# Optimization experiments

Hardware: AMD Instinct MI355X
Metric: run time of the kernel (lower is better)

## Reference

```python
import jax, jax.numpy as jnp
import numpy as np

P = 0.5          # dropout-style keep probability (wandb.config.probability)
Z = 1000         # number of Monte-Carlo normal draws in the original loop


def setup_inputs() -> dict:
    key = jax.random.key(0)
    k1, k2, k3 = jax.random.split(key, 3)
    B, D_in, H, C = 65536, 28 * 28, 256, 10
    x = jax.random.uniform(k1, (B, D_in), dtype=jnp.float32)          # pixel-like inputs in [0,1)
    W1 = jax.random.normal(k2, (H, D_in), dtype=jnp.float32) * 0.05   # fc1.weight
    W2 = jax.random.normal(k3, (C, H), dtype=jnp.float32) * 0.05      # fc2.weight
    return {"x": x, "W1": W1, "W2": W2}


def _mc_normal_layer(x, W, key):
    """Gaussian-dropout moment-propagation layer.

    Original torch code draws Z independent Normal(mean, std) samples and
    averages them, which is exactly Normal(mean, std / sqrt(Z)). We use the
    closed form: one eps draw instead of Z kernel launches.
    """
    mean = P * jnp.matmul(x, W.T)                                   # [B, out]
    var = P * (1.0 - P) * jnp.matmul(x * x, (W * W).T)              # [B, out]
    std = jnp.sqrt(var)
    eps = jax.random.normal(key, mean.shape, dtype=mean.dtype)
    return mean + std * (eps / jnp.sqrt(jnp.asarray(Z, mean.dtype)))


def reference(x, W1, W2):
    x = x.reshape(-1, 28 * 28)
    k1, k2 = jax.random.split(jax.random.key(42))
    h = jax.nn.relu(_mc_normal_layer(x, W1, k1))   # [B, H]
    out = _mc_normal_layer(h, W2, k2)              # [B, 10]
    return out
```

## Files before the change

### kernel.cpp

```cpp
#include <hip/hip_runtime.h>
#include <hip/hip_bf16.h>
#include <cstdint>


#define K_DIM 784
#define KP 800
#define N_HID 256
#define N_OUT 10
#define BM 64
#define NSTEP 25
#define WSQ_OFF (N_HID * KP)
#define W2_OFF (832 * 1024)
#define W2SQ 4096
#define H_OFF (1 << 20)
#define BM2 128

using short8 = __attribute__((ext_vector_type(8))) short;
using floatx4 = __attribute__((ext_vector_type(4))) float;
typedef uint16_t u16;

__host__ __device__ inline void threefry2x32(uint32_t k0, uint32_t k1,
                                             uint32_t x0, uint32_t x1,
                                             uint32_t& o0, uint32_t& o1) {
  uint32_t ks0 = k0, ks1 = k1, ks2 = k0 ^ k1 ^ 0x1BD11BDAu;
  x0 += ks0;
  x1 += ks1;
#define TFR(r) { x0 += x1; x1 = (x1 << (r)) | (x1 >> (32 - (r))); x1 ^= x0; }
  TFR(13) TFR(15) TFR(26) TFR(6)   x0 += ks1; x1 += ks2 + 1u;
  TFR(17) TFR(29) TFR(16) TFR(24)  x0 += ks2; x1 += ks0 + 2u;
  TFR(13) TFR(15) TFR(26) TFR(6)   x0 += ks0; x1 += ks1 + 3u;
  TFR(17) TFR(29) TFR(16) TFR(24)  x0 += ks1; x1 += ks2 + 4u;
  TFR(13) TFR(15) TFR(26) TFR(6)   x0 += ks2; x1 += ks0 + 5u;
#undef TFR
  o0 = x0;
  o1 = x1;
}

__device__ __forceinline__ float bits_to_normal(uint32_t bits) {
  const float lo = -0.99999994f;
  float u01 = __uint_as_float((bits >> 9) | 0x3F800000u) - 1.0f;
  float u = fmaxf(lo, u01 * 2.0f + lo);
  float w = -__logf((1.0f - u) * (1.0f + u));
  float p;
  if (w < 5.0f) {
    w -= 2.5f;
    p = 2.81022636e-08f;
    p = fmaf(p, w, 3.43273939e-07f);
    p = fmaf(p, w, -3.5233877e-06f);
    p = fmaf(p, w, -4.39150654e-06f);
    p = fmaf(p, w, 0.00021858087f);
    p = fmaf(p, w, -0.00125372503f);
    p = fmaf(p, w, -0.00417768164f);
    p = fmaf(p, w, 0.246640727f);
    p = fmaf(p, w, 1.50140941f);
  } else {
    w = sqrtf(w) - 3.0f;
    p = -0.000200214257f;
    p = fmaf(p, w, 0.000100950558f);
    p = fmaf(p, w, 0.00134934322f);
    p = fmaf(p, w, -0.00367342844f);
    p = fmaf(p, w, 0.00573950773f);
    p = fmaf(p, w, -0.0076224613f);
    p = fmaf(p, w, 0.00943887047f);
    p = fmaf(p, w, 1.00167406f);
    p = fmaf(p, w, 2.83297682f);
  }
  return 1.41421356f * (p * u);
}

__device__ __forceinline__ float eps_part(uint32_t ka, uint32_t kb, uint32_t i) {
  uint32_t o0, o1;
  threefry2x32(ka, kb, 0u, i, o0, o1);
  return bits_to_normal(o0 ^ o1);
}

__device__ __forceinline__ u16 cvt_bf16(float f) {
  union { __hip_bfloat16 h; u16 u; } c;
  c.h = __float2bfloat16(f);
  return c.u;
}

__device__ __forceinline__ float bf2f(u16 b) {
  return __uint_as_float((uint32_t)b << 16);
}

__global__ __launch_bounds__(256) void pack_w1(const float* __restrict__ W1,
                                               u16* __restrict__ bp) {
  const int col = blockIdx.x;
  for (int k = threadIdx.x; k < KP; k += 256) {
    float w = (k < K_DIM) ? W1[col * K_DIM + k] : 0.0f;
    bp[col * KP + k] = cvt_bf16(w);
    bp[WSQ_OFF + col * KP + k] = cvt_bf16(w * w);
  }
}

__global__ __launch_bounds__(256) void pack_w2(const float* __restrict__ W2,
                                               u16* __restrict__ w2p) {
#pragma unroll
  for (int i = 0; i < 16; ++i) {
    int g = threadIdx.x + i * 256;
    int col = g >> 8, k = g & 255;
    float w = (col < N_OUT) ? W2[col * N_HID + k] : 0.0f;
    w2p[g] = cvt_bf16(w);
    w2p[W2SQ + g] = cvt_bf16(w * w);
  }
}

__global__ __launch_bounds__(256, 4) void gemm1(
    const float* __restrict__ x, const u16* __restrict__ bp,
    u16* __restrict__ hws, uint32_t k1a, uint32_t k1b) {
  __shared__ u16 sA[2][2][BM * 32];

  const int tid = threadIdx.x;
  const int lane = tid & 63;
  const int l15 = lane & 15;
  const int lhal = lane >> 4;
  const int wn = tid >> 6;
  const int bid = blockIdx.x;
  const int gr0 = (bid >> 1) * BM;
  const int bc0 = (bid & 1) * 128;

  const int srow = tid >> 2;
  const int skq = (tid & 3) * 8;
  const float* xptr = x + (size_t)(gr0 + srow) * K_DIM + skq;
  const int sidx = (srow * 32 + skq) ^ ((srow & 7) << 3);

  const uint32_t boff0 = (uint32_t)(bc0 + wn * 32 + 0 * 16 + l15) * KP + (uint32_t)lhal * 8;
  const uint32_t boff1 = (uint32_t)(bc0 + wn * 32 + 1 * 16 + l15) * KP + (uint32_t)lhal * 8;

#define AIDX(i) ((((i * 16 + l15) * 32 + lhal * 8)) ^ (((i * 16 + l15) & 7) << 3))
  const int aidx0 = AIDX(0);
  const int aidx1 = AIDX(1);
  const int aidx2 = AIDX(2);
  const int aidx3 = AIDX(3);
#undef AIDX

#define DECL_ACC(i) \
  floatx4 am##i##0 = {0.f, 0.f, 0.f, 0.f}, am##i##1 = {0.f, 0.f, 0.f, 0.f}; \
  floatx4 av##i##0 = {0.f, 0.f, 0.f, 0.f}, av##i##1 = {0.f, 0.f, 0.f, 0.f};
  DECL_ACC(0) DECL_ACC(1) DECL_ACC(2) DECL_ACC(3)
#undef DECL_ACC

  short8 bm0P, bm1P, bv0P, bv1P;
  short8 bm0Q, bm1Q, bv0Q, bv1Q;
#define LOADB(S, KK) do { \
    const u16* bpk_ = bp + (KK); \
    bm0##S = *reinterpret_cast<const short8*>(&bpk_[boff0]); \
    bm1##S = *reinterpret_cast<const short8*>(&bpk_[boff1]); \
    bv0##S = *reinterpret_cast<const short8*>(&bpk_[WSQ_OFF + boff0]); \
    bv1##S = *reinterpret_cast<const short8*>(&bpk_[WSQ_OFF + boff1]); \
  } while (0)

  float4 q0, q1;
  auto loadX = [&](int kk) {
    if (kk + skq + 8 <= K_DIM) {
      q0 = *reinterpret_cast<const float4*>(xptr + kk);
      q1 = *reinterpret_cast<const float4*>(xptr + kk + 4);
    } else {
      q0 = make_float4(0.f, 0.f, 0.f, 0.f);
      q1 = make_float4(0.f, 0.f, 0.f, 0.f);
    }
  };
  auto writeA = [&](int buf) {
    short8 va, v2;
    va[0] = (short)cvt_bf16(q0.x); v2[0] = (short)cvt_bf16(q0.x * q0.x);
    va[1] = (short)cvt_bf16(q0.y); v2[1] = (short)cvt_bf16(q0.y * q0.y);
    va[2] = (short)cvt_bf16(q0.z); v2[2] = (short)cvt_bf16(q0.z * q0.z);
    va[3] = (short)cvt_bf16(q0.w); v2[3] = (short)cvt_bf16(q0.w * q0.w);
    va[4] = (short)cvt_bf16(q1.x); v2[4] = (short)cvt_bf16(q1.x * q1.x);
    va[5] = (short)cvt_bf16(q1.y); v2[5] = (short)cvt_bf16(q1.y * q1.y);
    va[6] = (short)cvt_bf16(q1.z); v2[6] = (short)cvt_bf16(q1.z * q1.z);
    va[7] = (short)cvt_bf16(q1.w); v2[7] = (short)cvt_bf16(q1.w * q1.w);
    *reinterpret_cast<short8*>(&sA[buf][0][sidx]) = va;
    *reinterpret_cast<short8*>(&sA[buf][1][sidx]) = v2;
  };

#define KSTEP(S_, CUR, NXT, LAST) do { \
    const int kk_ = (S_) * 32; \
    if (!(LAST)) { loadX(kk_ + 32); LOADB(NXT, kk_ + 32); } \
    const u16* sc0_ = &sA[(S_) & 1][0][0]; \
    const u16* sc1_ = &sA[(S_) & 1][1][0]; \
    { \
      const short8 af0_ = *reinterpret_cast<const short8*>(&sc0_[aidx0]); \
      const short8 ag0_ = *reinterpret_cast<const short8*>(&sc1_[aidx0]); \
      const short8 af1_ = *reinterpret_cast<const short8*>(&sc0_[aidx1]); \
      const short8 ag1_ = *reinterpret_cast<const short8*>(&sc1_[aidx1]); \
      const short8 af2_ = *reinterpret_cast<const short8*>(&sc0_[aidx2]); \
      const short8 ag2_ = *reinterpret_cast<const short8*>(&sc1_[aidx2]); \
      const short8 af3_ = *reinterpret_cast<const short8*>(&sc0_[aidx3]); \
      const short8 ag3_ = *reinterpret_cast<const short8*>(&sc1_[aidx3]); \
      am00 = __builtin_amdgcn_mfma_f32_16x16x32_bf16(af0_, bm0##CUR, am00, 0, 0, 0); \
      av00 = __builtin_amdgcn_mfma_f32_16x16x32_bf16(ag0_, bv0##CUR, av00, 0, 0, 0); \
      am01 = __builtin_amdgcn_mfma_f32_16x16x32_bf16(af0_, bm1##CUR, am01, 0, 0, 0); \
      av01 = __builtin_amdgcn_mfma_f32_16x16x32_bf16(ag0_, bv1##CUR, av01, 0, 0, 0); \
      am10 = __builtin_amdgcn_mfma_f32_16x16x32_bf16(af1_, bm0##CUR, am10, 0, 0, 0); \
      av10 = __builtin_amdgcn_mfma_f32_16x16x32_bf16(ag1_, bv0##CUR, av10, 0, 0, 0); \
      am11 = __builtin_amdgcn_mfma_f32_16x16x32_bf16(af1_, bm1##CUR, am11, 0, 0, 0); \
      av11 = __builtin_amdgcn_mfma_f32_16x16x32_bf16(ag1_, bv1##CUR, av11, 0, 0, 0); \
      am20 = __builtin_amdgcn_mfma_f32_16x16x32_bf16(af2_, bm0##CUR, am20, 0, 0, 0); \
      av20 = __builtin_amdgcn_mfma_f32_16x16x32_bf16(ag2_, bv0##CUR, av20, 0, 0, 0); \
      am21 = __builtin_amdgcn_mfma_f32_16x16x32_bf16(af2_, bm1##CUR, am21, 0, 0, 0); \
      av21 = __builtin_amdgcn_mfma_f32_16x16x32_bf16(ag2_, bv1##CUR, av21, 0, 0, 0); \
      am30 = __builtin_amdgcn_mfma_f32_16x16x32_bf16(af3_, bm0##CUR, am30, 0, 0, 0); \
      av30 = __builtin_amdgcn_mfma_f32_16x16x32_bf16(ag3_, bv0##CUR, av30, 0, 0, 0); \
      am31 = __builtin_amdgcn_mfma_f32_16x16x32_bf16(af3_, bm1##CUR, am31, 0, 0, 0); \
      av31 = __builtin_amdgcn_mfma_f32_16x16x32_bf16(ag3_, bv1##CUR, av31, 0, 0, 0); \
    } \
    if (!(LAST)) writeA(((S_) & 1) ^ 1); \
    __syncthreads(); \
  } while (0)

  loadX(0);
  writeA(0);
  LOADB(P, 0);
  __syncthreads();

  for (int s = 0; s < 24; s += 2) {
    KSTEP(s, P, Q, false);
    KSTEP(s + 1, Q, P, false);
  }
  KSTEP(24, P, Q, true);
#undef KSTEP
#undef LOADB

  const float INV = 0.031622776601683794f;
#define EPIG(AM, AV, G, I, J) do { \
    const int rl_ = I * 16 + lhal * 4 + (G); \
    const int c_ = bc0 + wn * 32 + J * 16 + l15; \
    float mean_ = 0.5f * (AM)[G]; \
    float sd_ = 0.5f * sqrtf((AV)[G]); \
    uint32_t idx_ = (uint32_t)(gr0 + rl_) * 256u + (uint32_t)c_; \
    float eps_ = eps_part(k1a, k1b, idx_); \
    float h_ = fmaxf(mean_ + sd_ * (eps_ * INV), 0.0f); \
    hws[(size_t)(gr0 + rl_) * 256 + c_] = cvt_bf16(h_); \
  } while (0)
#define EPI(i, j) do { \
    EPIG(am##i##j, av##i##j, 0, i, j); \
    EPIG(am##i##j, av##i##j, 1, i, j); \
    EPIG(am##i##j, av##i##j, 2, i, j); \
    EPIG(am##i##j, av##i##j, 3, i, j); \
  } while (0)
  EPI(0, 0); EPI(0, 1); EPI(1, 0); EPI(1, 1);
  EPI(2, 0); EPI(2, 1); EPI(3, 0); EPI(3, 1);
#undef EPI
#undef EPIG
}

__global__ __launch_bounds__(256, 4) void layer2(
    const u16* __restrict__ hws, const u16* __restrict__ w2p,
    float* __restrict__ out, uint32_t k2a, uint32_t k2b) {
  __shared__ u16 sH[2][BM2 * 32];

  const int tid = threadIdx.x;
  const int lane = tid & 63;
  const int l15 = lane & 15;
  const int lhal = lane >> 4;
  const int wv = tid >> 6;
  const int gr0 = blockIdx.x * BM2;

  const int srow = tid >> 1;
  const int sq = (tid & 1) * 16;
  const u16* hrow = hws + (size_t)(gr0 + srow) * 256 + sq;
  const int sidx0 = (srow * 32 + sq) ^ ((srow & 7) << 3);
  const int sidx1 = (srow * 32 + sq + 8) ^ ((srow & 7) << 3);

  const uint32_t boff = (uint32_t)l15 * 256 + (uint32_t)lhal * 8;

#define AIDX2(i) ((((wv * 32 + i * 16 + l15) * 32 + lhal * 8)) ^ (((wv * 32 + i * 16 + l15) & 7) << 3))
  const int aidx0 = AIDX2(0);
  const int aidx1 = AIDX2(1);
#undef AIDX2

  floatx4 am0 = {0.f, 0.f, 0.f, 0.f}, am1 = {0.f, 0.f, 0.f, 0.f};
  floatx4 av0 = {0.f, 0.f, 0.f, 0.f}, av1 = {0.f, 0.f, 0.f, 0.f};

  for (int s = 0; s < 8; ++s) {
    __syncthreads();
    const short8 c0 = *reinterpret_cast<const short8*>(&hrow[s * 32]);
    const short8 c1 = *reinterpret_cast<const short8*>(&hrow[s * 32 + 8]);
    short8 s0, s1;
#define SQE(D, S, E) { const float f_ = bf2f((u16)(S)[E]); (D)[E] = (short)cvt_bf16(f_ * f_); }
    SQE(s0, c0, 0) SQE(s0, c0, 1) SQE(s0, c0, 2) SQE(s0, c0, 3)
    SQE(s0, c0, 4) SQE(s0, c0, 5) SQE(s0, c0, 6) SQE(s0, c0, 7)
    SQE(s1, c1, 0) SQE(s1, c1, 1) SQE(s1, c1, 2) SQE(s1, c1, 3)
    SQE(s1, c1, 4) SQE(s1, c1, 5) SQE(s1, c1, 6) SQE(s1, c1, 7)
#undef SQE
    *reinterpret_cast<short8*>(&sH[0][sidx0]) = c0;
    *reinterpret_cast<short8*>(&sH[0][sidx1]) = c1;
    *reinterpret_cast<short8*>(&sH[1][sidx0]) = s0;
    *reinterpret_cast<short8*>(&sH[1][sidx1]) = s1;
    __syncthreads();

    const short8 bm = *reinterpret_cast<const short8*>(&w2p[boff + s * 32]);
    const short8 bv = *reinterpret_cast<const short8*>(&w2p[W2SQ + boff + s * 32]);
    const short8 af0 = *reinterpret_cast<const short8*>(&sH[0][aidx0]);
    const short8 af1 = *reinterpret_cast<const short8*>(&sH[0][aidx1]);
    const short8 ag0 = *reinterpret_cast<const short8*>(&sH[1][aidx0]);
    const short8 ag1 = *reinterpret_cast<const short8*>(&sH[1][aidx1]);
    am0 = __builtin_amdgcn_mfma_f32_16x16x32_bf16(af0, bm, am0, 0, 0, 0);
    av0 = __builtin_amdgcn_mfma_f32_16x16x32_bf16(ag0, bv, av0, 0, 0, 0);
    am1 = __builtin_amdgcn_mfma_f32_16x16x32_bf16(af1, bm, am1, 0, 0, 0);
    av1 = __builtin_amdgcn_mfma_f32_16x16x32_bf16(ag1, bv, av1, 0, 0, 0);
  }

  const float INV = 0.031622776601683794f;
  if (l15 < N_OUT) {
#define L2E(I, G) do { \
    const int row_ = gr0 + wv * 32 + I * 16 + lhal * 4 + (G); \
    float mean_ = 0.5f * am##I[G]; \
    float sd_ = 0.5f * sqrtf(av##I[G]); \
    float eps_ = eps_part(k2a, k2b, (uint32_t)row_ * 10u + (uint32_t)l15); \
    out[(size_t)row_ * 10 + l15] = mean_ + sd_ * (eps_ * INV); \
  } while (0)
    L2E(0, 0); L2E(0, 1); L2E(0, 2); L2E(0, 3);
    L2E(1, 0); L2E(1, 1); L2E(1, 2); L2E(1, 3);
#undef L2E
  }
}

extern "C" void kernel_launch(void* const* d_in, const int* in_sizes, int n_in,
                              void* d_out, int out_size, void* d_ws, size_t ws_size,
                              hipStream_t stream) {
  const float* x = (const float*)d_in[0];
  const float* W1 = (const float*)d_in[1];
  const float* W2 = (const float*)d_in[2];
  float* outp = (float*)d_out;
  u16* bp = (u16*)d_ws;
  u16* w2p = (u16*)((char*)d_ws + W2_OFF);
  u16* hws = (u16*)((char*)d_ws + H_OFF);

  uint32_t k1a, k1b, k2a, k2b;
  threefry2x32(0u, 42u, 0u, 0u, k1a, k1b);
  threefry2x32(0u, 42u, 0u, 1u, k2a, k2b);

  pack_w1<<<256, 256, 0, stream>>>(W1, bp);
  pack_w2<<<1, 256, 0, stream>>>(W2, w2p);
  gemm1<<<(65536 / BM) * 2, 256, 0, stream>>>(x, bp, hws, k1a, k1b);
  layer2<<<65536 / BM2, 256, 0, stream>>>(hws, w2p, outp, k2a, k2b);
}
```

Before: 158.8 us.

## Precompute layer-1 Gaussian noise in separate fp16 kernel before GEMM

Moves the threefry plus inverse-erf noise generation for the hidden layer out of the GEMM epilogue into a standalone rng1 kernel. That kernel packs the noise as fp16 into workspace in the same lane order the epilogue reads, so the GEMM only loads 16-byte vectors. The aim is to shorten the compute-heavy GEMM epilogue, at the cost of an extra launch and about 32 MB of extra memory traffic, and fp16 rounding of eps. The bf16 conversion is also replaced with manual round-to-nearest-even bit arithmetic. The old fused path is kept as a fallback when the workspace is too small.

```diff
diff --git a/kernel.cpp b/kernel.cpp
--- a/kernel.cpp
+++ b/kernel.cpp
@@ -1,5 +1,4 @@
 #include <hip/hip_runtime.h>
-#include <hip/hip_bf16.h>
 #include <cstdint>
 
 
@@ -7,15 +6,18 @@
 #define KP 800
 #define N_HID 256
 #define N_OUT 10
-#define BM 64
 #define NSTEP 25
 #define WSQ_OFF (N_HID * KP)
 #define W2_OFF (832 * 1024)
 #define W2SQ 4096
-#define H_OFF (1 << 20)
+#define EPS_OFF 1048576
+#define H_BIG 34603008
+#define H_SMALL 1048576
 #define BM2 128
 
 using short8 = __attribute__((ext_vector_type(8))) short;
+using half8 = __attribute__((ext_vector_type(8))) _Float16;
+using fp16x2 = __attribute__((ext_vector_type(2))) __fp16;
 using floatx4 = __attribute__((ext_vector_type(4))) float;
 typedef uint16_t u16;
 
@@ -75,13 +77,18 @@
 }
 
 __device__ __forceinline__ u16 cvt_bf16(float f) {
-  union { __hip_bfloat16 h; u16 u; } c;
-  c.h = __float2bfloat16(f);
-  return c.u;
+  uint32_t x = __float_as_uint(f);
+  return (u16)((x + 0x7FFFu + ((x >> 16) & 1u)) >> 16);
 }
 
 __device__ __forceinline__ float bf2f(u16 b) {
   return __uint_as_float((uint32_t)b << 16);
+}
+
+__device__ __forceinline__ int h2i(fp16x2 h) {
+  union { fp16x2 h; int i; } u;
+  u.h = h;
+  return u.i;
 }
 
 __global__ __launch_bounds__(256) void pack_w1(const float* __restrict__ W1,
@@ -106,18 +113,53 @@
   }
 }
 
-__global__ __launch_bounds__(256, 4) void gemm1(
-    const float* __restrict__ x, const u16* __restrict__ bp,
-    u16* __restrict__ hws, uint32_t k1a, uint32_t k1b) {
-  __shared__ u16 sA[2][2][BM * 32];
-
+__global__ __launch_bounds__(256, 8) void rng1(int4* __restrict__ ei4,
+                                               uint32_t k1a, uint32_t k1b) {
   const int tid = threadIdx.x;
   const int lane = tid & 63;
   const int l15 = lane & 15;
   const int lhal = lane >> 4;
   const int wn = tid >> 6;
   const int bid = blockIdx.x;
-  const int gr0 = (bid >> 1) * BM;
+  const int gr0 = (bid >> 1) * 64;
+  const int bc0 = (bid & 1) * 128;
+
+#define EIDX(D) ((uint32_t)(gr0 + ((D) >> 3) * 16 + lhal * 4 + ((D) & 3)) * 256u \
+                 + (uint32_t)(bc0 + wn * 32 + (((D) >> 2) & 1) * 16 + l15))
+#define PKE(P, D) const fp16x2 P = __builtin_amdgcn_cvt_pkrtz( \
+    eps_part(k1a, k1b, EIDX(D)), eps_part(k1a, k1b, EIDX((D) + 1)));
+  PKE(p0, 0)  PKE(p1, 2)  PKE(p2, 4)  PKE(p3, 6)
+  PKE(p4, 8)  PKE(p5, 10) PKE(p6, 12) PKE(p7, 14)
+  PKE(p8, 16) PKE(p9, 18) PKE(pa, 20) PKE(pb, 22)
+  PKE(pc, 24) PKE(pd, 26) PKE(pe, 28) PKE(pf, 30)
+#undef PKE
+#undef EIDX
+  int4 w0, w1, w2, w3;
+  w0.x = h2i(p0); w0.y = h2i(p1); w0.z = h2i(p2); w0.w = h2i(p3);
+  w1.x = h2i(p4); w1.y = h2i(p5); w1.z = h2i(p6); w1.w = h2i(p7);
+  w2.x = h2i(p8); w2.y = h2i(p9); w2.z = h2i(pa); w2.w = h2i(pb);
+  w3.x = h2i(pc); w3.y = h2i(pd); w3.z = h2i(pe); w3.w = h2i(pf);
+  int4* dst = ei4 + (size_t)bid * 1024 + tid;
+  dst[0] = w0;
+  dst[256] = w1;
+  dst[512] = w2;
+  dst[768] = w3;
+}
+
+template <int UE>
+__global__ __launch_bounds__(256, 4) void gemm1(
+    const float* __restrict__ x, const u16* __restrict__ bp,
+    u16* __restrict__ hws, const int4* __restrict__ ei4,
+    uint32_t k1a, uint32_t k1b) {
+  __shared__ u16 sA[2][2][64 * 32];
+
+  const int tid = threadIdx.x;
+  const int lane = tid & 63;
+  const int l15 = lane & 15;
+  const int lhal = lane >> 4;
+  const int wn = tid >> 6;
+  const int bid = blockIdx.x;
+  const int gr0 = (bid >> 1) * 64;
   const int bc0 = (bid & 1) * 128;
 
   const int srow = tid >> 2;
@@ -223,14 +265,23 @@
 #undef KSTEP
 #undef LOADB
 
+  half8 eA0, eA1, eA2, eA3;
+  if constexpr (UE) {
+    const int4* esrc = ei4 + (size_t)bid * 1024 + tid;
+    eA0 = *reinterpret_cast<const half8*>(&esrc[0]);
+    eA1 = *reinterpret_cast<const half8*>(&esrc[256]);
+    eA2 = *reinterpret_cast<const half8*>(&esrc[512]);
+    eA3 = *reinterpret_cast<const half8*>(&esrc[768]);
+  }
   const float INV = 0.031622776601683794f;
 #define EPIG(AM, AV, G, I, J) do { \
     const int rl_ = I * 16 + lhal * 4 + (G); \
     const int c_ = bc0 + wn * 32 + J * 16 + l15; \
     float mean_ = 0.5f * (AM)[G]; \
     float sd_ = 0.5f * sqrtf((AV)[G]); \
-    uint32_t idx_ = (uint32_t)(gr0 + rl_) * 256u + (uint32_t)c_; \
-    float eps_ = eps_part(k1a, k1b, idx_); \
+    float eps_; \
+    if constexpr (UE) eps_ = (float)(eA##I[(J) * 4 + (G)]); \
+    else eps_ = eps_part(k1a, k1b, (uint32_t)(gr0 + rl_) * 256u + (uint32_t)c_); \
     float h_ = fmaxf(mean_ + sd_ * (eps_ * INV), 0.0f); \
     hws[(size_t)(gr0 + rl_) * 256 + c_] = cvt_bf16(h_); \
   } while (0)
@@ -327,7 +378,6 @@
   float* outp = (float*)d_out;
   u16* bp = (u16*)d_ws;
   u16* w2p = (u16*)((char*)d_ws + W2_OFF);
-  u16* hws = (u16*)((char*)d_ws + H_OFF);
 
   uint32_t k1a, k1b, k2a, k2b;
   threefry2x32(0u, 42u, 0u, 0u, k1a, k1b);
@@ -335,6 +385,17 @@
 
   pack_w1<<<256, 256, 0, stream>>>(W1, bp);
   pack_w2<<<1, 256, 0, stream>>>(W2, w2p);
-  gemm1<<<(65536 / BM) * 2, 256, 0, stream>>>(x, bp, hws, k1a, k1b);
-  layer2<<<65536 / BM2, 256, 0, stream>>>(hws, w2p, outp, k2a, k2b);
-}
+
+  const size_t need = (size_t)H_BIG + 33554432ull;
+  if (ws_size >= need) {
+    int4* ei4 = (int4*)((char*)d_ws + EPS_OFF);
+    u16* hws = (u16*)((char*)d_ws + H_BIG);
+    rng1<<<2048, 256, 0, stream>>>(ei4, k1a, k1b);
+    gemm1<1><<<2048, 256, 0, stream>>>(x, bp, hws, ei4, k1a, k1b);
+    layer2<<<65536 / BM2, 256, 0, stream>>>(hws, w2p, outp, k2a, k2b);
+  } else {
+    u16* hws = (u16*)((char*)d_ws + H_SMALL);
+    gemm1<0><<<2048, 256, 0, stream>>>(x, bp, hws, nullptr, k1a, k1b);
+    layer2<<<65536 / BM2, 256, 0, stream>>>(hws, w2p, outp, k2a, k2b);
+  }
+}
```

New measurement: 207.5 us. 1.31x slower.
